# Optimization experiments

Hardware: AMD Instinct MI355X
Metric: run time of the kernel (lower is better)

The kernel has to match this reference:

```python
import jax, jax.numpy as jnp
import numpy as np

# batches, users-per-batch (max_user_num), servers-per-batch (max_server_num), dims
B, U, S, DU, DS, H = 64, 256, 64, 16, 16, 256
DEG_S, DEG_U = 8, 16
NU, NS = B * U, B * S
IN_DIM = U * DU + S * DS  # 5120


def setup_inputs() -> dict:
    key = jax.random.key(0)
    ks = jax.random.split(key, 12)
    x_user = jax.random.normal(ks[0], (NU, DU), jnp.float32)
    x_server = jax.random.normal(ks[1], (NS, DS), jnp.float32)
    # within-batch edges: user u in batch u//U connects to servers/users of same batch
    src_u2s = jnp.repeat(jnp.arange(NU), DEG_S)
    dst_u2s = (src_u2s // U) * S + jax.random.randint(ks[2], (NU * DEG_S,), 0, S)
    src_u2u = jnp.repeat(jnp.arange(NU), DEG_U)
    dst_u2u = (src_u2u // U) * U + jax.random.randint(ks[3], (NU * DEG_U,), 0, U)

    def lin(k, i, o):
        return jax.random.normal(k, (i, o), jnp.float32) * 0.02

    params = dict(
        oW1=lin(ks[4], IN_DIM, H), ob1=jnp.zeros((H,), jnp.float32),
        oW2=lin(ks[5], H, H), ob2=jnp.zeros((H,), jnp.float32),
        oW3=lin(ks[6], H, 2), ob3=jnp.zeros((2,), jnp.float32),
        sW1=lin(ks[7], IN_DIM, H), sb1=jnp.zeros((H,), jnp.float32),
        sW2=lin(ks[8], H, H), sb2=jnp.zeros((H,), jnp.float32),
        sW3=lin(ks[9], H, S), sb3=jnp.zeros((S,), jnp.float32),
    )
    return dict(x_user=x_user, x_server=x_server,
                src_u2s=src_u2s, dst_u2s=dst_u2s,
                src_u2u=src_u2u, dst_u2u=dst_u2u, **params)


def _mlp3(x, W1, b1, W2, b2, W3, b3):
    h = jax.nn.relu(x @ W1 + b1)
    h = jax.nn.sigmoid(h @ W2 + b2)
    return h @ W3 + b3


def reference(x_user, x_server, src_u2s, dst_u2s, src_u2u, dst_u2u,
              oW1, ob1, oW2, ob2, oW3, ob3, sW1, sb1, sW2, sb2, sW3, sb3):
    # scatter neighbor features into per-user dense observation slots
    # (edges are within-batch, so dst % S / dst % U is the local slot index,
    #  identical to the original global-offset scatter + batch mask)
    server_obs = (jnp.zeros((NU, S, DS), x_server.dtype)
                  .at[src_u2s, dst_u2s % S].set(x_server[dst_u2s]))
    user_obs = (jnp.zeros((NU, U, DU), x_user.dtype)
                .at[src_u2u, dst_u2u % U].set(x_user[dst_u2u]))
    feats = jnp.concatenate([server_obs.reshape(B, U, S * DS),
                             user_obs.reshape(B, U, U * DU)], axis=-1)  # [B,U,IN_DIM]
    offloading_probs = jax.nn.softmax(
        _mlp3(feats, oW1, ob1, oW2, ob2, oW3, ob3), axis=-1)  # [B,U,2]
    sel_logits = _mlp3(feats, sW1, sb1, sW2, sb2, sW3, sb3)   # [B,U,S]
    # -inf mask: 0 only at (user, server) pairs connected by a u2s edge
    non_probs = (jnp.full((NU, S), -jnp.inf, jnp.float32)
                 .at[src_u2s, dst_u2s % S].set(0.0)
                 .reshape(B, U, S))
    selection_probs = jax.nn.softmax(sel_logits + non_probs, axis=-1)
    return offloading_probs, selection_probs
```

## Files before the change

### kernel.cpp

```cpp
#include <hip/hip_runtime.h>
#include <hip/hip_bf16.h>
#include <math.h>
#include <cstdint>

#define NUSER 16384
#define BB    64
#define UU    256
#define SSLOT 64
#define HD    256
#define KTOT  320
#define DEGS  8
#define DEGU  16

typedef __attribute__((ext_vector_type(8))) short short8;
typedef __attribute__((ext_vector_type(4))) float f32x4;

static __device__ __forceinline__ __hip_bfloat16 f2b(float x) { return __float2bfloat16(x); }
static __device__ __forceinline__ unsigned pack2(float x, float y) {
  union { __hip_bfloat16 h[2]; unsigned u; } cv;
  cv.h[0] = f2b(x); cv.h[1] = f2b(y);
  return cv.u;
}

__global__ __launch_bounds__(256) void k_prep_pq(
    const int* __restrict__ dst_u2s, const int* __restrict__ dst_u2u,
    const float* __restrict__ oW2, const float* __restrict__ sW2,
    const float* __restrict__ sW3,
    const float* __restrict__ xu, const float* __restrict__ xs,
    const float* __restrict__ oW1, const float* __restrict__ sW1,
    unsigned long long* __restrict__ connS, unsigned* __restrict__ MSUW,
    __hip_bfloat16* __restrict__ W2F_o, __hip_bfloat16* __restrict__ W2F_s,
    __hip_bfloat16* __restrict__ W3F_s,
    __hip_bfloat16* __restrict__ P_o, __hip_bfloat16* __restrict__ P_s,
    __hip_bfloat16* __restrict__ Q_o, __hip_bfloat16* __restrict__ Q_s) {
  const int t = threadIdx.x;
  if (blockIdx.y == 0) {
    const int blk = blockIdx.x;
    if (blk < 64) {
      const int u = blk * 256 + t;
      unsigned long long ms = 0ull;
      #pragma unroll
      for (int i = 0; i < DEGS; ++i) ms |= 1ull << (dst_u2s[u * DEGS + i] & 63);
      connS[u] = ms;
      unsigned long long m0 = 0, m1 = 0, m2 = 0, m3 = 0;
      #pragma unroll
      for (int i = 0; i < DEGU; ++i) {
        int slot = dst_u2u[u * DEGU + i] & 255;
        unsigned long long bit = 1ull << (slot & 63);
        int w = slot >> 6;
        if (w == 0) m0 |= bit; else if (w == 1) m1 |= bit;
        else if (w == 2) m2 |= bit; else m3 |= bit;
      }
      unsigned* mw = MSUW + (size_t)u * 10;
      uint2* mw2 = (uint2*)mw;
      mw2[0] = make_uint2((unsigned)ms, (unsigned)(ms >> 32));
      mw2[1] = make_uint2((unsigned)m0, (unsigned)(m0 >> 32));
      mw2[2] = make_uint2((unsigned)m1, (unsigned)(m1 >> 32));
      mw2[3] = make_uint2((unsigned)m2, (unsigned)(m2 >> 32));
      mw2[4] = make_uint2((unsigned)m3, (unsigned)(m3 >> 32));
      {
        const int n = blk;
        const int ks = t >> 5, hi = (t >> 3) & 3, e = t & 7;
        const int lane = hi * 16 + (n & 15);
        const size_t idx = (size_t)((((n >> 4) * 8 + ks) * 64 + lane)) * 8 + e;
        W3F_s[idx] = f2b(sW3[(ks * 32 + hi * 8 + e) * SSLOT + n]);
      }
    } else {
      const int n = blk - 64;
      const int ks = t >> 5, hi = (t >> 3) & 3, e = t & 7;
      const int lane = hi * 16 + (n & 15);
      const size_t idx = (size_t)((((n >> 4) * 8 + ks) * 64 + lane)) * 8 + e;
      const int k = ks * 32 + hi * 8 + e;
      W2F_o[idx] = f2b(oW2[k * HD + n]);
      W2F_s[idx] = f2b(sW2[k * HD + n]);
    }
    return;
  }
  const int wg = blockIdx.x;
  const int b0 = (blockIdx.y - 1) * 8;
  __shared__ float lx[8 * 16];
  const bool isS = wg < SSLOT;
  const int slot = isS ? wg : wg - SSLOT;
  if (t < 8 * 16) {
    int b = b0 + (t >> 4), d = t & 15;
    lx[t] = isS ? xs[(b * SSLOT + slot) * 16 + d] : xu[(b * UU + slot) * 16 + d];
  }
  __syncthreads();
  float wo[16], wsv[16];
  const int rbase = isS ? slot * 16 : SSLOT * 16 + slot * 16;
  #pragma unroll
  for (int d = 0; d < 16; ++d) {
    wo[d] = oW1[(rbase + d) * HD + t];
    wsv[d] = sW1[(rbase + d) * HD + t];
  }
  __hip_bfloat16* Ro = isS ? P_o : Q_o;
  __hip_bfloat16* Rs = isS ? P_s : Q_s;
  const int rows = isS ? SSLOT : UU;
  #pragma unroll
  for (int bi = 0; bi < 8; ++bi) {
    float ao = 0.f, as = 0.f;
    #pragma unroll
    for (int q = 0; q < 4; ++q) {
      float4 x4 = *(const float4*)&lx[bi * 16 + q * 4];
      ao = fmaf(x4.x, wo[q*4+0], ao); as = fmaf(x4.x, wsv[q*4+0], as);
      ao = fmaf(x4.y, wo[q*4+1], ao); as = fmaf(x4.y, wsv[q*4+1], as);
      ao = fmaf(x4.z, wo[q*4+2], ao); as = fmaf(x4.z, wsv[q*4+2], as);
      ao = fmaf(x4.w, wo[q*4+3], ao); as = fmaf(x4.w, wsv[q*4+3], as);
    }
    Ro[((b0 + bi) * rows + slot) * HD + t] = f2b(ao);
    Rs[((b0 + bi) * rows + slot) * HD + t] = f2b(as);
  }
}

__global__ __launch_bounds__(256) void k_tr(
    const __hip_bfloat16* __restrict__ P_o, const __hip_bfloat16* __restrict__ P_s,
    const __hip_bfloat16* __restrict__ Q_o, const __hip_bfloat16* __restrict__ Q_s,
    __hip_bfloat16* __restrict__ PQT_o, __hip_bfloat16* __restrict__ PQT_s) {
  const int b = blockIdx.x, mlp = blockIdx.y, nc = blockIdx.z;
  const int n0 = nc * 64;
  const int t = threadIdx.x;
  const __hip_bfloat16* P = mlp ? P_s : P_o;
  const __hip_bfloat16* Q = mlp ? Q_s : Q_o;
  __hip_bfloat16* PQT = mlp ? PQT_s : PQT_o;
  __shared__ __align__(16) short lds[64 * 72];
  for (int kt = 0; kt < 5; ++kt) {
    const __hip_bfloat16* src = (kt == 0) ? (P + (size_t)(b * SSLOT) * HD)
                                          : (Q + (size_t)(b * UU + (kt - 1) * 64) * HD);
    const int kout = (kt == 0) ? 0 : 64 + (kt - 1) * 64;
    #pragma unroll
    for (int i = 0; i < 2; ++i) {
      int c = t + i * 256;
      int row = c >> 3, cc = c & 7;
      *(short8*)&lds[row * 72 + cc * 8] =
          *(const short8*)(src + (size_t)row * HD + n0 + cc * 8);
    }
    __syncthreads();
    #pragma unroll
    for (int i = 0; i < 2; ++i) {
      int c = t + i * 256;
      int nrow = c >> 3, kc = c & 7;
      short8 v;
      #pragma unroll
      for (int e = 0; e < 8; ++e) v[e] = lds[(kc * 8 + e) * 72 + nrow];
      *(short8*)(PQT + (size_t)(b * 256 + n0 + nrow) * KTOT + kout + kc * 8) = v;
    }
    __syncthreads();
  }
}

__global__ __launch_bounds__(256) void k_h1(
    const unsigned* __restrict__ MSUW,
    const __hip_bfloat16* __restrict__ PQT_o, const __hip_bfloat16* __restrict__ PQT_s,
    const float* __restrict__ ob1, const float* __restrict__ sb1,
    __hip_bfloat16* __restrict__ h1o, __hip_bfloat16* __restrict__ h1s) {
  const int b = blockIdx.x >> 1, uh = blockIdx.x & 1;
  const int mlp = blockIdx.y, nh = blockIdx.z;
  const int n0 = nh * 128;
  const int t = threadIdx.x;
  const __hip_bfloat16* PQT = mlp ? PQT_s : PQT_o;
  const float* b1 = mlp ? sb1 : ob1;
  __hip_bfloat16* h1 = mlp ? h1s : h1o;

  __shared__ __align__(16) char smem[48128];
  short* pan = (short*)smem;
  unsigned* mskL = (unsigned*)(smem + 43008);

  {
    const unsigned* g = MSUW + (size_t)(b * 256 + uh * 128) * 10;
    #pragma unroll
    for (int i = 0; i < 5; ++i) mskL[t + 256 * i] = g[t + 256 * i];
  }
  const int lane = t & 63, w = t >> 6;
  const int lo = lane & 15, hi = lane >> 4;
  f32x4 acc[2][8] = {};
  for (int kc = 0; kc < 2; ++kc) {
    if (kc) __syncthreads();
    {
      const int r = t >> 1, c4 = t & 1;
      const __hip_bfloat16* src = PQT + (size_t)(b * 256 + n0 + r) * KTOT + kc * 160;
      #pragma unroll
      for (int i = 0; i < 10; ++i) {
        int cc = c4 + 2 * i;
        *(short8*)&pan[r * 168 + cc * 8] = *(const short8*)(src + cc * 8);
      }
    }
    __syncthreads();
    #pragma unroll
    for (int kt2 = 0; kt2 < 5; ++kt2) {
      const int kt = kc * 5 + kt2;
      short8 af[2], bf[8];
      #pragma unroll
      for (int rb = 0; rb < 2; ++rb) {
        int lu = w * 32 + rb * 16 + lo;
        unsigned m = mskL[lu * 10 + kt];
        unsigned by = (m >> (hi * 8)) & 0xFFu;
        union { unsigned u[4]; short8 s; } cv;
        cv.u[0] = ((by & 1u)  ? 0x3F80u : 0u) | ((by & 2u)   ? 0x3F800000u : 0u);
        cv.u[1] = ((by & 4u)  ? 0x3F80u : 0u) | ((by & 8u)   ? 0x3F800000u : 0u);
        cv.u[2] = ((by & 16u) ? 0x3F80u : 0u) | ((by & 32u)  ? 0x3F800000u : 0u);
        cv.u[3] = ((by & 64u) ? 0x3F80u : 0u) | ((by & 128u) ? 0x3F800000u : 0u);
        af[rb] = cv.s;
      }
      #pragma unroll
      for (int cb = 0; cb < 8; ++cb) {
        int n = cb * 16 + lo;
        bf[cb] = *(const short8*)&pan[n * 168 + (kt2 * 4 + hi) * 8];
      }
      #pragma unroll
      for (int rb = 0; rb < 2; ++rb)
        #pragma unroll
        for (int cb = 0; cb < 8; ++cb)
          acc[rb][cb] = __builtin_amdgcn_mfma_f32_16x16x32_bf16(af[rb], bf[cb], acc[rb][cb], 0, 0, 0);
    }
  }
  #pragma unroll
  for (int cb = 0; cb < 8; ++cb) {
    int n = cb * 16 + lo;
    float bv = b1[n0 + n];
    #pragma unroll
    for (int rb = 0; rb < 2; ++rb) {
      #pragma unroll
      for (int j = 0; j < 4; ++j) {
        int u = b * 256 + uh * 128 + w * 32 + rb * 16 + hi * 4 + j;
        h1[(size_t)u * HD + n0 + n] = f2b(fmaxf(acc[rb][cb][j] + bv, 0.f));
      }
    }
  }
}

__global__ __launch_bounds__(256) void k_heads(
    const __hip_bfloat16* __restrict__ h1o, const __hip_bfloat16* __restrict__ h1s,
    const __hip_bfloat16* __restrict__ W2F_o, const __hip_bfloat16* __restrict__ W2F_s,
    const float* __restrict__ ob2, const float* __restrict__ sb2,
    const float* __restrict__ oW3, const float* __restrict__ ob3,
    const __hip_bfloat16* __restrict__ W3F_s, const float* __restrict__ sb3,
    const unsigned long long* __restrict__ connS,
    float* __restrict__ out) {
  const int mlp = blockIdx.y;
  const int x = blockIdx.x;
  const int blk = (x & 7) * 32 + (x >> 3);
  const int u0 = blk * 64;
  const int t = threadIdx.x, lane = t & 63, wid = t >> 6;
  const int lo = lane & 15, hi = lane >> 4;

  const __hip_bfloat16* A   = mlp ? h1s : h1o;
  const __hip_bfloat16* W2F = mlp ? W2F_s : W2F_o;
  const float* b2 = mlp ? sb2 : ob2;

  __shared__ __align__(16) char lds[32768 + 2048];
  short* As = (short*)lds;
  float* part = (float*)(lds + 32768);

  #pragma unroll
  for (int i = 0; i < 8; ++i) {
    int c = t + i * 256;
    int row = c >> 5, cc = c & 31;
    *(short8*)&As[row * 256 + (cc ^ (row & 7)) * 8] =
        *(const short8*)(A + (size_t)(u0 + row) * HD + cc * 8);
  }
  __syncthreads();

  f32x4 acc2[4][4] = {};
  #pragma unroll
  for (int ks = 0; ks < 8; ++ks) {
    short8 af[4], bf[4];
    #pragma unroll
    for (int rb = 0; rb < 4; ++rb) {
      int row = rb * 16 + lo;
      int ca = ks * 4 + hi;
      af[rb] = *(const short8*)&As[row * 256 + (ca ^ (row & 7)) * 8];
    }
    #pragma unroll
    for (int cb = 0; cb < 4; ++cb) {
      bf[cb] = *(const short8*)(W2F + (size_t)((((wid * 4 + cb) * 8 + ks) * 64 + lane)) * 8);
    }
    #pragma unroll
    for (int rb = 0; rb < 4; ++rb)
      #pragma unroll
      for (int cb = 0; cb < 4; ++cb)
        acc2[rb][cb] = __builtin_amdgcn_mfma_f32_16x16x32_bf16(af[rb], bf[cb], acc2[rb][cb], 0, 0, 0);
  }
  __syncthreads();

  if (mlp == 0) {
    float p0[4][4] = {}, p1[4][4] = {};
    #pragma unroll
    for (int cb = 0; cb < 4; ++cb) {
      int n = wid * 64 + cb * 16 + lo;
      float bs = b2[n], w0 = oW3[2 * n], w1 = oW3[2 * n + 1];
      #pragma unroll
      for (int rb = 0; rb < 4; ++rb)
        #pragma unroll
        for (int j = 0; j < 4; ++j) {
          float sig = 1.0f / (1.0f + __expf(-(acc2[rb][cb][j] + bs)));
          p0[rb][j] = fmaf(sig, w0, p0[rb][j]);
          p1[rb][j] = fmaf(sig, w1, p1[rb][j]);
        }
    }
    #pragma unroll
    for (int rb = 0; rb < 4; ++rb)
      #pragma unroll
      for (int j = 0; j < 4; ++j) {
        #pragma unroll
        for (int off = 1; off < 16; off <<= 1) {
          p0[rb][j] += __shfl_xor(p0[rb][j], off, 64);
          p1[rb][j] += __shfl_xor(p1[rb][j], off, 64);
        }
        if (lo == 0) {
          int row = rb * 16 + hi * 4 + j;
          part[wid * 128 + row * 2 + 0] = p0[rb][j];
          part[wid * 128 + row * 2 + 1] = p1[rb][j];
        }
      }
    __syncthreads();
    if (t < 64) {
      float q0 = part[t * 2] + part[128 + t * 2] + part[256 + t * 2] + part[384 + t * 2] + ob3[0];
      float q1 = part[t * 2 + 1] + part[128 + t * 2 + 1] + part[256 + t * 2 + 1] + part[384 + t * 2 + 1] + ob3[1];
      float m2 = fmaxf(q0, q1);
      float e0 = __expf(q0 - m2), e1 = __expf(q1 - m2);
      float iv = 1.0f / (e0 + e1);
      float2 r; r.x = e0 * iv; r.y = e1 * iv;
      *(float2*)(out + (size_t)(u0 + t) * 2) = r;
    }
  } else {
    short* sel = As;
    #pragma unroll
    for (int cb = 0; cb < 4; ++cb) {
      int n = wid * 64 + cb * 16 + lo;
      float bs = b2[n];
      #pragma unroll
      for (int rb = 0; rb < 4; ++rb)
        #pragma unroll
        for (int j = 0; j < 4; ++j) {
          int row = rb * 16 + hi * 4 + j;
          float sig = 1.0f / (1.0f + __expf(-(acc2[rb][cb][j] + bs)));
          sel[row * 256 + ((n >> 3) ^ (row & 7)) * 8 + (n & 7)] = (short)pack2(sig, 0.f);
        }
    }
    __syncthreads();
    f32x4 acc3[4] = {};
    #pragma unroll
    for (int ks = 0; ks < 8; ++ks) {
      int row = wid * 16 + lo;
      int ca = ks * 4 + hi;
      short8 af = *(const short8*)&sel[row * 256 + (ca ^ (row & 7)) * 8];
      #pragma unroll
      for (int cb = 0; cb < 4; ++cb) {
        short8 bf = *(const short8*)(W3F_s + (size_t)(((cb * 8 + ks) * 64 + lane)) * 8);
        acc3[cb] = __builtin_amdgcn_mfma_f32_16x16x32_bf16(af, bf, acc3[cb], 0, 0, 0);
      }
    }
    float sb3n[4];
    #pragma unroll
    for (int cb = 0; cb < 4; ++cb) sb3n[cb] = sb3[cb * 16 + lo];
    const int ubase = u0 + wid * 16 + hi * 4;
    #pragma unroll
    for (int j = 0; j < 4; ++j) {
      unsigned long long m = connS[ubase + j];
      float v[4]; bool ok[4];
      float mx = -INFINITY;
      #pragma unroll
      for (int cb = 0; cb < 4; ++cb) {
        int n = cb * 16 + lo;
        ok[cb] = (m >> n) & 1ull;
        v[cb] = ok[cb] ? (acc3[cb][j] + sb3n[cb]) : -INFINITY;
        mx = fmaxf(mx, v[cb]);
      }
      #pragma unroll
      for (int off = 1; off < 16; off <<= 1) mx = fmaxf(mx, __shfl_xor(mx, off, 64));
      float e[4], ssum = 0.f;
      #pragma unroll
      for (int cb = 0; cb < 4; ++cb) {
        e[cb] = ok[cb] ? __expf(v[cb] - mx) : 0.f;
        ssum += e[cb];
      }
      #pragma unroll
      for (int off = 1; off < 16; off <<= 1) ssum += __shfl_xor(ssum, off, 64);
      float iv = 1.0f / ssum;
      #pragma unroll
      for (int cb = 0; cb < 4; ++cb) {
        int n = cb * 16 + lo;
        out[(size_t)NUSER * 2 + (size_t)(ubase + j) * SSLOT + n] = e[cb] * iv;
      }
    }
  }
}

extern "C" void kernel_launch(void* const* d_in, const int* in_sizes, int n_in,
                              void* d_out, int out_size, void* d_ws, size_t ws_size,
                              hipStream_t stream) {
  const float* x_user   = (const float*)d_in[0];
  const float* x_server = (const float*)d_in[1];
  const int*   dst_u2s  = (const int*)d_in[3];
  const int*   dst_u2u  = (const int*)d_in[5];
  const float* oW1 = (const float*)d_in[6];
  const float* ob1 = (const float*)d_in[7];
  const float* oW2 = (const float*)d_in[8];
  const float* ob2 = (const float*)d_in[9];
  const float* oW3 = (const float*)d_in[10];
  const float* ob3 = (const float*)d_in[11];
  const float* sW1 = (const float*)d_in[12];
  const float* sb1 = (const float*)d_in[13];
  const float* sW2 = (const float*)d_in[14];
  const float* sb2 = (const float*)d_in[15];
  const float* sW3 = (const float*)d_in[16];
  const float* sb3 = (const float*)d_in[17];

  char* ws = (char*)d_ws;
  unsigned long long* connS = (unsigned long long*)(ws + 0);
  unsigned*       MSUW  = (unsigned*)(ws + 131072);
  __hip_bfloat16* P_o  = (__hip_bfloat16*)(ws + 786432);
  __hip_bfloat16* P_s  = (__hip_bfloat16*)(ws + 2883584);
  __hip_bfloat16* Q_o  = (__hip_bfloat16*)(ws + 4980736);
  __hip_bfloat16* Q_s  = (__hip_bfloat16*)(ws + 13369344);
  __hip_bfloat16* PQT_o = (__hip_bfloat16*)(ws + 21757952);
  __hip_bfloat16* PQT_s = (__hip_bfloat16*)(ws + 32243712);
  __hip_bfloat16* h1o  = (__hip_bfloat16*)(ws + 42729472);
  __hip_bfloat16* h1s  = (__hip_bfloat16*)(ws + 51118080);
  __hip_bfloat16* W2F_o = (__hip_bfloat16*)(ws + 59506688);
  __hip_bfloat16* W2F_s = (__hip_bfloat16*)(ws + 59637760);
  __hip_bfloat16* W3F_s = (__hip_bfloat16*)(ws + 59768832);
  float* out = (float*)d_out;

  k_prep_pq<<<dim3(320, 9), 256, 0, stream>>>(
      dst_u2s, dst_u2u, oW2, sW2, sW3, x_user, x_server, oW1, sW1,
      connS, MSUW, W2F_o, W2F_s, W3F_s, P_o, P_s, Q_o, Q_s);
  k_tr<<<dim3(64, 2, 4), 256, 0, stream>>>(P_o, P_s, Q_o, Q_s, PQT_o, PQT_s);
  k_h1<<<dim3(128, 2, 2), 256, 0, stream>>>(MSUW, PQT_o, PQT_s, ob1, sb1, h1o, h1s);
  k_heads<<<dim3(256, 2), 256, 0, stream>>>(h1o, h1s, W2F_o, W2F_s, ob2, sb2,
                                            oW3, ob3, W3F_s, sb3, connS, out);
}
```

Baseline: 56.82 us.

## Fuse P/Q transpose into first-layer GEMM kernel via LDS transpose

Removes the separate transpose kernel that wrote a transposed PQT buffer to global memory. The h1 kernel now loads the P/Q tiles directly, transposes each 64-row chunk in LDS, and feeds the MFMA from there. This saves one kernel launch and a full global write and read of the PQT buffers. In exchange each h1 block redoes the transpose work, and the K loop now has five chunks with two barriers each instead of two chunks.

```diff
diff --git a/kernel.cpp b/kernel.cpp
--- a/kernel.cpp
+++ b/kernel.cpp
@@ -112,58 +112,25 @@
   }
 }
 
-__global__ __launch_bounds__(256) void k_tr(
+__global__ __launch_bounds__(256) void k_h1f(
+    const unsigned* __restrict__ MSUW,
     const __hip_bfloat16* __restrict__ P_o, const __hip_bfloat16* __restrict__ P_s,
     const __hip_bfloat16* __restrict__ Q_o, const __hip_bfloat16* __restrict__ Q_s,
-    __hip_bfloat16* __restrict__ PQT_o, __hip_bfloat16* __restrict__ PQT_s) {
-  const int b = blockIdx.x, mlp = blockIdx.y, nc = blockIdx.z;
-  const int n0 = nc * 64;
-  const int t = threadIdx.x;
-  const __hip_bfloat16* P = mlp ? P_s : P_o;
-  const __hip_bfloat16* Q = mlp ? Q_s : Q_o;
-  __hip_bfloat16* PQT = mlp ? PQT_s : PQT_o;
-  __shared__ __align__(16) short lds[64 * 72];
-  for (int kt = 0; kt < 5; ++kt) {
-    const __hip_bfloat16* src = (kt == 0) ? (P + (size_t)(b * SSLOT) * HD)
-                                          : (Q + (size_t)(b * UU + (kt - 1) * 64) * HD);
-    const int kout = (kt == 0) ? 0 : 64 + (kt - 1) * 64;
-    #pragma unroll
-    for (int i = 0; i < 2; ++i) {
-      int c = t + i * 256;
-      int row = c >> 3, cc = c & 7;
-      *(short8*)&lds[row * 72 + cc * 8] =
-          *(const short8*)(src + (size_t)row * HD + n0 + cc * 8);
-    }
-    __syncthreads();
-    #pragma unroll
-    for (int i = 0; i < 2; ++i) {
-      int c = t + i * 256;
-      int nrow = c >> 3, kc = c & 7;
-      short8 v;
-      #pragma unroll
-      for (int e = 0; e < 8; ++e) v[e] = lds[(kc * 8 + e) * 72 + nrow];
-      *(short8*)(PQT + (size_t)(b * 256 + n0 + nrow) * KTOT + kout + kc * 8) = v;
-    }
-    __syncthreads();
-  }
-}
-
-__global__ __launch_bounds__(256) void k_h1(
-    const unsigned* __restrict__ MSUW,
-    const __hip_bfloat16* __restrict__ PQT_o, const __hip_bfloat16* __restrict__ PQT_s,
     const float* __restrict__ ob1, const float* __restrict__ sb1,
     __hip_bfloat16* __restrict__ h1o, __hip_bfloat16* __restrict__ h1s) {
   const int b = blockIdx.x >> 1, uh = blockIdx.x & 1;
   const int mlp = blockIdx.y, nh = blockIdx.z;
   const int n0 = nh * 128;
   const int t = threadIdx.x;
-  const __hip_bfloat16* PQT = mlp ? PQT_s : PQT_o;
+  const __hip_bfloat16* P = mlp ? P_s : P_o;
+  const __hip_bfloat16* Q = mlp ? Q_s : Q_o;
   const float* b1 = mlp ? sb1 : ob1;
   __hip_bfloat16* h1 = mlp ? h1s : h1o;
 
-  __shared__ __align__(16) char smem[48128];
-  short* pan = (short*)smem;
-  unsigned* mskL = (unsigned*)(smem + 43008);
+  __shared__ __align__(16) char smem[17408 + 18432 + 5120];
+  short* buf = (short*)smem;
+  short* pan = (short*)(smem + 17408);
+  unsigned* mskL = (unsigned*)(smem + 35840);
 
   {
     const unsigned* g = MSUW + (size_t)(b * 256 + uh * 128) * 10;
@@ -173,21 +140,34 @@
   const int lane = t & 63, w = t >> 6;
   const int lo = lane & 15, hi = lane >> 4;
   f32x4 acc[2][8] = {};
-  for (int kc = 0; kc < 2; ++kc) {
+  for (int kc = 0; kc < 5; ++kc) {
     if (kc) __syncthreads();
     {
-      const int r = t >> 1, c4 = t & 1;
-      const __hip_bfloat16* src = PQT + (size_t)(b * 256 + n0 + r) * KTOT + kc * 160;
-      #pragma unroll
-      for (int i = 0; i < 10; ++i) {
-        int cc = c4 + 2 * i;
-        *(short8*)&pan[r * 168 + cc * 8] = *(const short8*)(src + cc * 8);
+      const __hip_bfloat16* base = (kc == 0)
+          ? (P + (size_t)(b * SSLOT) * HD + n0)
+          : (Q + (size_t)(b * UU + (kc - 1) * 64) * HD + n0);
+      #pragma unroll
+      for (int i = 0; i < 4; ++i) {
+        int idx = t + i * 256;
+        int r = idx >> 4, cc = idx & 15;
+        *(short8*)&buf[r * 136 + cc * 8] =
+            *(const short8*)(base + (size_t)r * HD + cc * 8);
       }
     }
     __syncthreads();
     #pragma unroll
-    for (int kt2 = 0; kt2 < 5; ++kt2) {
-      const int kt = kc * 5 + kt2;
+    for (int i = 0; i < 4; ++i) {
+      int idx = t + i * 256;
+      int n = idx >> 3, k8 = idx & 7;
+      short8 v;
+      #pragma unroll
+      for (int e = 0; e < 8; ++e) v[e] = buf[(k8 * 8 + e) * 136 + n];
+      *(short8*)&pan[n * 72 + k8 * 8] = v;
+    }
+    __syncthreads();
+    #pragma unroll
+    for (int kt2 = 0; kt2 < 2; ++kt2) {
+      const int kt = kc * 2 + kt2;
       short8 af[2], bf[8];
       #pragma unroll
       for (int rb = 0; rb < 2; ++rb) {
@@ -204,7 +184,7 @@
       #pragma unroll
       for (int cb = 0; cb < 8; ++cb) {
         int n = cb * 16 + lo;
-        bf[cb] = *(const short8*)&pan[n * 168 + (kt2 * 4 + hi) * 8];
+        bf[cb] = *(const short8*)&pan[n * 72 + (kt2 * 4 + hi) * 8];
       }
       #pragma unroll
       for (int rb = 0; rb < 2; ++rb)
@@ -413,20 +393,18 @@
   __hip_bfloat16* P_s  = (__hip_bfloat16*)(ws + 2883584);
   __hip_bfloat16* Q_o  = (__hip_bfloat16*)(ws + 4980736);
   __hip_bfloat16* Q_s  = (__hip_bfloat16*)(ws + 13369344);
-  __hip_bfloat16* PQT_o = (__hip_bfloat16*)(ws + 21757952);
-  __hip_bfloat16* PQT_s = (__hip_bfloat16*)(ws + 32243712);
-  __hip_bfloat16* h1o  = (__hip_bfloat16*)(ws + 42729472);
-  __hip_bfloat16* h1s  = (__hip_bfloat16*)(ws + 51118080);
-  __hip_bfloat16* W2F_o = (__hip_bfloat16*)(ws + 59506688);
-  __hip_bfloat16* W2F_s = (__hip_bfloat16*)(ws + 59637760);
-  __hip_bfloat16* W3F_s = (__hip_bfloat16*)(ws + 59768832);
+  __hip_bfloat16* h1o  = (__hip_bfloat16*)(ws + 21757952);
+  __hip_bfloat16* h1s  = (__hip_bfloat16*)(ws + 30146560);
+  __hip_bfloat16* W2F_o = (__hip_bfloat16*)(ws + 38535168);
+  __hip_bfloat16* W2F_s = (__hip_bfloat16*)(ws + 38666240);
+  __hip_bfloat16* W3F_s = (__hip_bfloat16*)(ws + 38797312);
   float* out = (float*)d_out;
 
   k_prep_pq<<<dim3(320, 9), 256, 0, stream>>>(
       dst_u2s, dst_u2u, oW2, sW2, sW3, x_user, x_server, oW1, sW1,
       connS, MSUW, W2F_o, W2F_s, W3F_s, P_o, P_s, Q_o, Q_s);
-  k_tr<<<dim3(64, 2, 4), 256, 0, stream>>>(P_o, P_s, Q_o, Q_s, PQT_o, PQT_s);
-  k_h1<<<dim3(128, 2, 2), 256, 0, stream>>>(MSUW, PQT_o, PQT_s, ob1, sb1, h1o, h1s);
+  k_h1f<<<dim3(128, 2, 2), 256, 0, stream>>>(MSUW, P_o, P_s, Q_o, Q_s,
+                                             ob1, sb1, h1o, h1s);
   k_heads<<<dim3(256, 2), 256, 0, stream>>>(h1o, h1s, W2F_o, W2F_s, ob2, sb2,
                                             oW3, ob3, W3F_s, sb3, connS, out);
 }
```

Measured after the change: 57.64 us. Within noise of the previous version (+1.4%).
